# Kernel tuning notes

Hardware: AMD Instinct MI355X
Metric: run time of the kernel (lower is better)

## Reference

```python
import jax, jax.numpy as jnp
import numpy as np

D_MODEL = 768
H = 24            # nheads = d_inner / headdim
P = 64            # headdim
N = 64            # d_state (Mamba2Simple default)
DIN = 2 * D_MODEL             # expand=2 -> 1536
CONV_DIM = DIN + 2 * N        # 1664
DPROJ = 2 * DIN + 2 * N + H   # 3260
N_WRAPS = 8                   # 4 MambaFlipFlop layers x 2 MambaWrap each
IMG = 64 * 64
CHUNK = 128
EPS = 1e-5


def layer_norm(x, w, b):
    mu = jnp.mean(x, -1, keepdims=True)
    var = jnp.mean((x - mu) ** 2, -1, keepdims=True)
    return (x - mu) * jax.lax.rsqrt(var + EPS) * w + b


def segsum_exp(a):
    # a: [..., L] -> exp of segment sums, lower triangular (diag = 1)
    ac = jnp.cumsum(a, -1)
    d = ac[..., :, None] - ac[..., None, :]
    Lm = a.shape[-1]
    mask = jnp.tril(jnp.ones((Lm, Lm), bool))
    return jnp.exp(jnp.where(mask, d, -jnp.inf))


def ssd(X, A, Bm, Cm):
    # Chunked SSD (Mamba2). X:[b,t,h,p] (=x*dt), A:[b,t,h] (=dt*A_head),
    # Bm/Cm:[b,t,n] (ngroups=1, broadcast over heads).
    b, t, h, p = X.shape
    pad = (-t) % CHUNK
    X = jnp.pad(X, ((0, 0), (0, pad), (0, 0), (0, 0)))
    A = jnp.pad(A, ((0, 0), (0, pad), (0, 0)))
    Bm = jnp.pad(Bm, ((0, 0), (0, pad), (0, 0)))
    Cm = jnp.pad(Cm, ((0, 0), (0, pad), (0, 0)))
    c = (t + pad) // CHUNK
    X = X.reshape(b, c, CHUNK, h, p)
    A = A.reshape(b, c, CHUNK, h).transpose(0, 3, 1, 2)     # [b,h,c,l]
    Bm = Bm.reshape(b, c, CHUNK, N)
    Cm = Cm.reshape(b, c, CHUNK, N)
    Acs = jnp.cumsum(A, -1)                                  # [b,h,c,l]
    # intra-chunk (diagonal) block
    Lmat = segsum_exp(A)                                     # [b,h,c,l,l]
    G = jnp.einsum('bcln,bcsn->bcls', Cm, Bm)                # [b,c,l,s]
    M = G[:, None] * Lmat                                    # [b,h,c,l,s]
    Yd = jnp.einsum('bhcls,bcshp->bclhp', M, X)
    # chunk final states
    dec_st = jnp.exp(Acs[..., -1:] - Acs)                    # [b,h,c,l]
    states = jnp.einsum('bcln,bhcl,bclhp->bchpn', Bm, dec_st, X)
    states = jnp.concatenate([jnp.zeros_like(states[:, :1]), states], 1)
    chunk_sum = jnp.pad(Acs[..., -1], ((0, 0), (0, 0), (1, 0)))  # [b,h,c+1]
    dec_ch = segsum_exp(chunk_sum)                           # [b,h,c+1,c+1]
    states = jnp.einsum('bhzc,bchpn->bzhpn', dec_ch, states)[:, :-1]
    # state -> output (off-diagonal contribution)
    Yo = jnp.einsum('bcln,bchpn,bhcl->bclhp', Cm, states, jnp.exp(Acs))
    Y = (Yd + Yo).reshape(b, c * CHUNK, h, p)
    return Y[:, :t]


def mamba2(x, in_w, cw, cb, dtb, A_log, Dp, rmsw, ow):
    b, t, _ = x.shape
    zxbcdt = jnp.einsum('btd,ed->bte', x, in_w)              # [b,t,DPROJ]
    z = zxbcdt[..., :DIN]
    xBC = zxbcdt[..., DIN:DIN + CONV_DIM]
    dt = jax.nn.softplus(zxbcdt[..., -H:] + dtb)             # [b,t,H]
    # causal depthwise conv1d (kernel 4, pad left 3) + silu
    xBC = jax.lax.conv_general_dilated(
        xBC.transpose(0, 2, 1), cw, (1,), [(3, 0)],
        feature_group_count=CONV_DIM,
        dimension_numbers=('NCH', 'OIH', 'NCH')) + cb[None, :, None]
    xBC = jax.nn.silu(xBC).transpose(0, 2, 1)
    xh = xBC[..., :DIN].reshape(b, t, H, P)
    Bm = xBC[..., DIN:DIN + N]
    Cm = xBC[..., DIN + N:]
    A = -jnp.exp(A_log)                                      # [H]
    y = ssd(xh * dt[..., None], dt * A, Bm, Cm)
    y = y + Dp[None, None, :, None] * xh                     # D skip
    y = y.reshape(b, t, DIN)
    y = y * jax.nn.silu(z)                                   # gated RMSNorm
    y = y * jax.lax.rsqrt(jnp.mean(y * y, -1, keepdims=True) + EPS) * rmsw
    return jnp.einsum('btd,od->bto', y, ow)


def _model(im8, im64, from_rgb_w, from_rgb_b, to_rgb_w, to_rgb_b, s0, suffix,
           norm0_w, norm0_b, in_proj_w, conv1d_w, conv1d_b, dt_bias, A_log, Dp,
           rms_w, out_proj_w, ln_w, ln_b, lnc_w, lnc_b, conv2d_w, conv2d_b):
    b = im8.shape[0]
    e8 = im8 @ from_rgb_w.T + from_rgb_b                     # [b,64,D]
    z = e8.reshape(b, 8, 8, D_MODEL)                         # zoom 8x8 -> 64x64
    z = jnp.repeat(jnp.repeat(z, 8, 1), 8, 2).reshape(b, IMG, D_MODEL) + suffix
    x = jnp.concatenate([jnp.broadcast_to(s0, (b, 1, D_MODEL)), e8, z], 1)
    x = layer_norm(x, norm0_w, norm0_b)                      # [b,4161,D]

    def wrap(x, i):
        r = x
        h = layer_norm(x, ln_w[i], ln_b[i])
        h = mamba2(h, in_proj_w[i], conv1d_w[i], conv1d_b[i], dt_bias[i],
                   A_log[i], Dp[i], rms_w[i], out_proj_w[i])
        img = layer_norm(h[:, -IMG:], lnc_w[i], lnc_b[i]).reshape(b, 64, 64, D_MODEL)
        img = jax.lax.conv_general_dilated(
            img, conv2d_w[i], (1, 1), 'SAME',
            dimension_numbers=('NHWC', 'HWIO', 'NHWC')) + conv2d_b[i]
        h = jnp.concatenate([h[:, :-IMG], img.reshape(b, IMG, D_MODEL)], 1)
        return r + h

    def swap(x):  # reverse last IMG tokens (MambaFlipFlop.swap_order)
        return jnp.concatenate([x[:, :-IMG], jnp.flip(x[:, -IMG:], 1)], 1)

    for l in range(4):
        x = swap(wrap(x, 2 * l))
        x = swap(wrap(x, 2 * l + 1))
    y_hat = x[:, -IMG:] @ to_rgb_w.T + to_rgb_b              # [b,4096,3]
    loss = jnp.mean((y_hat - im64) ** 2)
    return y_hat, loss


def setup_inputs():
    key = jax.random.key(0)
    ks = jax.random.split(key, 16)
    rn = lambda k, s, sc=0.02: jax.random.normal(k, s, jnp.float32) * sc
    u = jax.random.uniform(ks[10], (N_WRAPS, H), minval=1e-3, maxval=0.1)
    return dict(
        im8=jax.random.normal(ks[0], (1, 64, 3), jnp.float32),
        im64=jax.random.normal(ks[1], (1, IMG, 3), jnp.float32),
        from_rgb_w=rn(ks[2], (D_MODEL, 3), 0.2),
        from_rgb_b=jnp.zeros((D_MODEL,), jnp.float32),
        to_rgb_w=rn(ks[3], (3, D_MODEL)),
        to_rgb_b=jnp.zeros((3,), jnp.float32),
        s0=rn(ks[4], (1, 1, D_MODEL), 1.0),
        suffix=rn(ks[5], (IMG, D_MODEL)),
        norm0_w=jnp.ones((D_MODEL,), jnp.float32),
        norm0_b=jnp.zeros((D_MODEL,), jnp.float32),
        in_proj_w=rn(ks[6], (N_WRAPS, DPROJ, D_MODEL)),
        conv1d_w=rn(ks[7], (N_WRAPS, CONV_DIM, 1, 4), 0.2),
        conv1d_b=jnp.zeros((N_WRAPS, CONV_DIM), jnp.float32),
        dt_bias=jnp.log(jnp.expm1(u)),
        A_log=jnp.log(jax.random.uniform(ks[11], (N_WRAPS, H), minval=1.0, maxval=16.0)),
        Dp=jnp.ones((N_WRAPS, H), jnp.float32),
        rms_w=jnp.ones((N_WRAPS, DIN), jnp.float32),
        out_proj_w=rn(ks[8], (N_WRAPS, D_MODEL, DIN)),
        ln_w=jnp.ones((N_WRAPS, D_MODEL), jnp.float32),
        ln_b=jnp.zeros((N_WRAPS, D_MODEL), jnp.float32),
        lnc_w=jnp.ones((N_WRAPS, D_MODEL), jnp.float32),
        lnc_b=jnp.zeros((N_WRAPS, D_MODEL), jnp.float32),
        conv2d_w=rn(ks[9], (N_WRAPS, 5, 5, D_MODEL, D_MODEL)),
        conv2d_b=jnp.zeros((N_WRAPS, D_MODEL), jnp.float32),
    )


def reference(im8, im64, from_rgb_w, from_rgb_b, to_rgb_w, to_rgb_b, s0, suffix,
              norm0_w, norm0_b, in_proj_w, conv1d_w, conv1d_b, dt_bias, A_log, Dp,
              rms_w, out_proj_w, ln_w, ln_b, lnc_w, lnc_b, conv2d_w, conv2d_b):
    return _model(im8, im64, from_rgb_w, from_rgb_b, to_rgb_w, to_rgb_b, s0, suffix,
                  norm0_w, norm0_b, in_proj_w, conv1d_w, conv1d_b, dt_bias, A_log, Dp,
                  rms_w, out_proj_w, ln_w, ln_b, lnc_w, lnc_b, conv2d_w, conv2d_b)
```

## Files before the change

kernel.cpp:

```cpp
#include <hip/hip_runtime.h>

#define D_MODEL 768
#define NH 24
#define HP 64
#define NSTATE 64
#define DIN 1536
#define CONV_DIM 1664
#define DPROJ 3224
#define TLEN 4161
#define IMG 4096
#define NCHUNK 33
#define CHUNK 128
#define TPAD (NCHUNK*CHUNK)
#define KCONV 19200

__device__ __forceinline__ float softplusf(float x) { return x > 20.f ? x : log1pf(expf(x)); }
__device__ __forceinline__ float siluf(float x) { return x / (1.f + expf(-x)); }

typedef __attribute__((ext_vector_type(8))) short short8v;
typedef __attribute__((ext_vector_type(4))) float ffrag;

__device__ __forceinline__ void splitf(float x, short& h, short& l) {
  unsigned u = __float_as_uint(x);
  unsigned r = (u + 0x7FFFu + ((u >> 16) & 1u)) & 0xFFFF0000u;
  h = (short)(r >> 16);
  float hf = __uint_as_float(r);
  float lof = x - hf;
  unsigned u2 = __float_as_uint(lof);
  unsigned r2 = u2 + 0x7FFFu + ((u2 >> 16) & 1u);
  l = (short)(r2 >> 16);
}

__device__ __forceinline__ void mfma_bf16(ffrag& c, short8v a, short8v b) {
  c = __builtin_amdgcn_mfma_f32_16x16x32_bf16(a, b, c, 0, 0, 0);
}

__global__ void e8_kernel(const float* __restrict__ im8, const float* __restrict__ w,
                          const float* __restrict__ b, float* __restrict__ e8) {
  int gid = blockIdx.x * blockDim.x + threadIdx.x;
  if (gid >= 64 * D_MODEL) return;
  int j = gid / D_MODEL, d = gid % D_MODEL;
  float acc = b[d];
  for (int c = 0; c < 3; c++) acc += im8[j * 3 + c] * w[d * 3 + c];
  e8[gid] = acc;
}

__global__ void build_x_kernel(const float* __restrict__ e8, const float* __restrict__ s0,
                               const float* __restrict__ suffix, float* __restrict__ out) {
  for (int gid = blockIdx.x * blockDim.x + threadIdx.x; gid < TLEN * D_MODEL;
       gid += gridDim.x * blockDim.x) {
    int t = gid / D_MODEL, d = gid % D_MODEL;
    float v;
    if (t == 0) v = s0[d];
    else if (t < 65) v = e8[(t - 1) * D_MODEL + d];
    else {
      int i = t - 65;
      int r = i >> 6, c = i & 63;
      v = e8[((r >> 3) * 8 + (c >> 3)) * D_MODEL + d] + suffix[(size_t)i * D_MODEL + d];
    }
    out[gid] = v;
  }
}

__global__ __launch_bounds__(256) void ln_kernel(const float* __restrict__ in,
                                                 const float* __restrict__ w, const float* __restrict__ b,
                                                 float* __restrict__ outf,
                                                 short* __restrict__ oh, short* __restrict__ ol,
                                                 int rows) {
  int r = blockIdx.x;
  if (r >= rows) return;
  const float* row = in + (size_t)r * D_MODEL;
  __shared__ float red[256];
  int tid = threadIdx.x;
  float v0 = row[tid], v1 = row[tid + 256], v2 = row[tid + 512];
  red[tid] = v0 + v1 + v2;
  __syncthreads();
  for (int o = 128; o; o >>= 1) { if (tid < o) red[tid] += red[tid + o]; __syncthreads(); }
  float mu = red[0] / (float)D_MODEL;
  __syncthreads();
  float d0 = v0 - mu, d1 = v1 - mu, d2 = v2 - mu;
  red[tid] = d0 * d0 + d1 * d1 + d2 * d2;
  __syncthreads();
  for (int o = 128; o; o >>= 1) { if (tid < o) red[tid] += red[tid + o]; __syncthreads(); }
  float inv = rsqrtf(red[0] / (float)D_MODEL + 1e-5f);
  float r0 = d0 * inv * w[tid] + b[tid];
  float r1 = d1 * inv * w[tid + 256] + b[tid + 256];
  float r2 = d2 * inv * w[tid + 512] + b[tid + 512];
  if (oh) {
    size_t base = (size_t)r * D_MODEL;
    short h, l;
    splitf(r0, h, l); oh[base + tid] = h; ol[base + tid] = l;
    splitf(r1, h, l); oh[base + tid + 256] = h; ol[base + tid + 256] = l;
    splitf(r2, h, l); oh[base + tid + 512] = h; ol[base + tid + 512] = l;
  } else {
    float* orow = outf + (size_t)r * D_MODEL;
    orow[tid] = r0; orow[tid + 256] = r1; orow[tid + 512] = r2;
  }
}

__global__ void split_mat_kernel(const float* __restrict__ src, short* __restrict__ hi,
                                 short* __restrict__ lo, int n) {
  for (int i = blockIdx.x * blockDim.x + threadIdx.x; i < n; i += gridDim.x * blockDim.x) {
    short h, l; splitf(src[i], h, l);
    hi[i] = h; lo[i] = l;
  }
}

__global__ __launch_bounds__(256) void split_convw_kernel(const float* __restrict__ W,
                                                          short* __restrict__ hi,
                                                          short* __restrict__ lo) {
  __shared__ float t[32][33];
  int tap = blockIdx.x;
  int ic0 = blockIdx.y * 32, oc0 = blockIdx.z * 32;
  int tid = threadIdx.x;
  #pragma unroll
  for (int e = 0; e < 4; e++) {
    int idx = tid + e * 256;
    int r = idx >> 5, c = idx & 31;
    t[r][c] = W[((size_t)tap * 768 + ic0 + r) * 768 + oc0 + c];
  }
  __syncthreads();
  #pragma unroll
  for (int e = 0; e < 4; e++) {
    int idx = tid + e * 256;
    int r = idx & 31, c = idx >> 5;
    short h, l; splitf(t[r][c], h, l);
    size_t o = (size_t)(oc0 + c) * KCONV + (size_t)tap * 768 + ic0 + r;
    hi[o] = h; lo[o] = l;
  }
}

template<int CONV>
__global__ __launch_bounds__(256, 2) void mm_bf16(
    const short* __restrict__ Ah, const short* __restrict__ Al,
    const short* __restrict__ Bh, const short* __restrict__ Bl,
    float* __restrict__ C, float* __restrict__ Cpart,
    int M, int N, int K, int ldb) {
  __shared__ __align__(16) short AsH[128 * 64];
  __shared__ __align__(16) short AsL[128 * 64];
  __shared__ __align__(16) short BsH[128 * 64];
  __shared__ __align__(16) short BsL[128 * 64];
  const int bm = blockIdx.x * 128;
  const int bn = blockIdx.y * 128;
  const int tid = threadIdx.x;
  const int lane = tid & 63;
  const int wid = tid >> 6;
  const int wm = (wid >> 1) * 64, wn = (wid & 1) * 64;
  const int lm = lane & 15, lk = lane >> 4;
  const int tap0 = CONV ? blockIdx.z * 5 : 0;
  const int nsteps = CONV ? 5 * 12 : K / 64;
  float* Cout = C;
  if (CONV && blockIdx.z > 0) Cout = Cpart + (size_t)(blockIdx.z - 1) * IMG * D_MODEL;
  const short8v ZV = {0, 0, 0, 0, 0, 0, 0, 0};

  short8v sAh[4], sAl[4], sBh[4], sBl[4];
  int s_row[4], s_kc[4];
  #pragma unroll
  for (int e = 0; e < 4; e++) { int id = tid + e * 256; s_row[e] = id >> 3; s_kc[e] = id & 7; }

  auto stage = [&](int step) {
    int k0, tap = 0;
    if (CONV) { tap = tap0 + step / 12; k0 = (step % 12) * 64; }
    else k0 = step * 64;
    #pragma unroll
    for (int e = 0; e < 4; e++) {
      int row = s_row[e], kc = s_kc[e];
      bool av; size_t aoff;
      if (CONV) {
        int px = bm + row;
        int r = (px >> 6) + tap / 5 - 2;
        int c = (px & 63) + tap % 5 - 2;
        av = (r >= 0 && r < 64 && c >= 0 && c < 64);
        aoff = (size_t)(r * 64 + c) * 768 + k0 + kc * 8;
      } else {
        int gm = bm + row;
        av = gm < M;
        aoff = (size_t)gm * K + k0 + kc * 8;
      }
      sAh[e] = av ? *(const short8v*)(Ah + aoff) : ZV;
      sAl[e] = av ? *(const short8v*)(Al + aoff) : ZV;
      int gn = bn + row;
      bool bv = gn < N;
      size_t boff = (size_t)gn * ldb + (CONV ? tap * 768 : 0) + k0 + kc * 8;
      sBh[e] = bv ? *(const short8v*)(Bh + boff) : ZV;
      sBl[e] = bv ? *(const short8v*)(Bl + boff) : ZV;
    }
  };

  auto lds_write = [&]() {
    #pragma unroll
    for (int e = 0; e < 4; e++) {
      int row = s_row[e];
      int off = row * 64 + ((s_kc[e] ^ (row & 7)) * 8);
      *(short8v*)(AsH + off) = sAh[e];
      *(short8v*)(AsL + off) = sAl[e];
      *(short8v*)(BsH + off) = sBh[e];
      *(short8v*)(BsL + off) = sBl[e];
    }
  };

  ffrag acc[4][4];
  const ffrag FZ = {0.f, 0.f, 0.f, 0.f};
  #pragma unroll
  for (int i = 0; i < 4; i++)
    #pragma unroll
    for (int j = 0; j < 4; j++) acc[i][j] = FZ;

  auto compute = [&]() {
    #pragma unroll
    for (int ks = 0; ks < 2; ks++) {
      short8v ahf[4], alf[4], bhf[4], blf[4];
      #pragma unroll
      for (int i = 0; i < 4; i++) {
        int ra = wm + i * 16 + lm;
        int oa = ra * 64 + (((lk + 4 * ks) ^ (ra & 7)) * 8);
        ahf[i] = *(const short8v*)(AsH + oa);
        alf[i] = *(const short8v*)(AsL + oa);
        int rb = wn + i * 16 + lm;
        int ob = rb * 64 + (((lk + 4 * ks) ^ (rb & 7)) * 8);
        bhf[i] = *(const short8v*)(BsH + ob);
        blf[i] = *(const short8v*)(BsL + ob);
      }
      #pragma unroll
      for (int i = 0; i < 4; i++)
        #pragma unroll
        for (int j = 0; j < 4; j++) {
          mfma_bf16(acc[i][j], ahf[i], bhf[j]);
          mfma_bf16(acc[i][j], ahf[i], blf[j]);
          mfma_bf16(acc[i][j], alf[i], bhf[j]);
        }
    }
  };

  stage(0);
  lds_write();
  __syncthreads();
  for (int step = 0; step < nsteps; ++step) {
    bool more = step + 1 < nsteps;
    if (more) stage(step + 1);
    compute();
    __syncthreads();
    if (more) { lds_write(); __syncthreads(); }
  }

  #pragma unroll
  for (int i = 0; i < 4; i++) {
    #pragma unroll
    for (int r = 0; r < 4; r++) {
      int row = bm + wm + i * 16 + lk * 4 + r;
      if (row >= M) continue;
      #pragma unroll
      for (int j = 0; j < 4; j++) {
        int col = bn + wn + j * 16 + lm;
        if (col < N) Cout[(size_t)row * N + col] = acc[i][j][r];
      }
    }
  }
}

__global__ void conv_reduce_kernel(float* __restrict__ dst, const float* __restrict__ part,
                                   const float* __restrict__ bias) {
  for (int gid = blockIdx.x * blockDim.x + threadIdx.x; gid < IMG * D_MODEL;
       gid += gridDim.x * blockDim.x) {
    float s = dst[gid] + bias[gid % D_MODEL];
    #pragma unroll
    for (int p = 0; p < 4; p++) s += part[(size_t)p * IMG * D_MODEL + gid];
    dst[gid] = s;
  }
}

__global__ void conv1d_kernel(const float* __restrict__ zx, const float* __restrict__ cw,
                              const float* __restrict__ cb, float* __restrict__ xBC) {
  for (int gid = blockIdx.x * blockDim.x + threadIdx.x; gid < TLEN * CONV_DIM;
       gid += gridDim.x * blockDim.x) {
    int t = gid / CONV_DIM, ch = gid % CONV_DIM;
    float acc = cb[ch];
    #pragma unroll
    for (int k = 0; k < 4; k++) {
      int tt = t - 3 + k;
      if (tt >= 0) acc += zx[(size_t)tt * DPROJ + DIN + ch] * cw[ch * 4 + k];
    }
    xBC[gid] = siluf(acc);
  }
}

__global__ void dt_kernel(const float* __restrict__ zx, const float* __restrict__ dt_bias,
                          float* __restrict__ dt) {
  for (int gid = blockIdx.x * blockDim.x + threadIdx.x; gid < TLEN * NH;
       gid += gridDim.x * blockDim.x) {
    int t = gid / NH, h = gid % NH;
    float v = zx[(size_t)t * DPROJ + DPROJ - NH + h] + dt_bias[h];
    dt[gid] = softplusf(v);
  }
}

__global__ void acs_kernel(const float* __restrict__ dt, const float* __restrict__ A_log,
                           float* __restrict__ Acs, float* __restrict__ csum) {
  int gid = blockIdx.x * blockDim.x + threadIdx.x;
  if (gid >= NCHUNK * NH) return;
  int c = gid / NH, h = gid % NH;
  float A = -expf(A_log[h]);
  float acc = 0.f;
  for (int l = 0; l < CHUNK; l++) {
    int t = c * CHUNK + l;
    float a = (t < TLEN) ? dt[(size_t)t * NH + h] * A : 0.f;
    acc += a;
    Acs[(size_t)(c * CHUNK + l) * NH + h] = acc;
  }
  csum[c * NH + h] = acc;
}

__global__ __launch_bounds__(256) void chunk_state_kernel(const float* __restrict__ xBC,
                                                          const float* __restrict__ dt,
                                                          const float* __restrict__ Acs,
                                                          const float* __restrict__ csum,
                                                          float* __restrict__ cstate) {
  int c = blockIdx.x, h = blockIdx.y;
  __shared__ float Bs[CHUNK][NSTATE];
  __shared__ float Xs[CHUNK][HP];
  int tid = threadIdx.x;
  float cs = csum[c * NH + h];
  for (int idx = tid; idx < CHUNK * 64; idx += 256) {
    int l = idx >> 6, n = idx & 63;
    int t = c * CHUNK + l;
    if (t < TLEN) {
      float a = Acs[(size_t)t * NH + h];
      Bs[l][n] = xBC[(size_t)t * CONV_DIM + DIN + n];
      Xs[l][n] = xBC[(size_t)t * CONV_DIM + h * HP + n] * dt[(size_t)t * NH + h] * expf(cs - a);
    } else { Bs[l][n] = 0.f; Xs[l][n] = 0.f; }
  }
  __syncthreads();
  int pt = (tid >> 4) * 4, nt = (tid & 15) * 4;
  float acc[4][4] = {};
  for (int l = 0; l < CHUNK; l++) {
    float xv[4], bv[4];
    #pragma unroll
    for (int i = 0; i < 4; i++) xv[i] = Xs[l][pt + i];
    #pragma unroll
    for (int j = 0; j < 4; j++) bv[j] = Bs[l][nt + j];
    #pragma unroll
    for (int i = 0; i < 4; i++)
      #pragma unroll
      for (int j = 0; j < 4; j++) acc[i][j] += xv[i] * bv[j];
  }
  size_t base = (((size_t)c * NH) + h) * 64 * 64;
  for (int i = 0; i < 4; i++)
    for (int j = 0; j < 4; j++)
      cstate[base + (size_t)(pt + i) * 64 + nt + j] = acc[i][j];
}

__global__ __launch_bounds__(256) void state_scan_kernel(const float* __restrict__ cstate,
                                                         const float* __restrict__ csum,
                                                         float* __restrict__ sstate) {
  int h = blockIdx.x;
  int tid = threadIdx.x;
  float S[16];
  #pragma unroll
  for (int j = 0; j < 16; j++) S[j] = 0.f;
  for (int z = 0; z < NCHUNK; z++) {
    size_t base = (((size_t)z * NH) + h) * 4096;
    float dec = expf(csum[z * NH + h]);
    #pragma unroll
    for (int j = 0; j < 16; j++) {
      int idx = j * 256 + tid;
      sstate[base + idx] = S[j];
      S[j] = S[j] * dec + cstate[base + idx];
    }
  }
}

__global__ __launch_bounds__(256, 1) void ssd_y_kernel(const float* __restrict__ xBC,
                                                       const float* __restrict__ dt,
                                                       const float* __restrict__ Acs,
                                                       const float* __restrict__ sstate,
                                                       const float* __restrict__ Dp,
                                                       float* __restrict__ y) {
  int c = blockIdx.x, h = blockIdx.y;
  __shared__ float Cs[CHUNK][NSTATE];
  __shared__ float Bx[CHUNK][NSTATE];
  __shared__ float Gm[CHUNK][CHUNK];
  __shared__ float Ash[CHUNK];
  int tid = threadIdx.x;
  for (int idx = tid; idx < CHUNK * 64; idx += 256) {
    int l = idx >> 6, n = idx & 63;
    int t = c * CHUNK + l;
    bool v = t < TLEN;
    Cs[l][n] = v ? xBC[(size_t)t * CONV_DIM + DIN + NSTATE + n] : 0.f;
    Bx[l][n] = v ? xBC[(size_t)t * CONV_DIM + DIN + n] : 0.f;
  }
  if (tid < CHUNK) Ash[tid] = Acs[(size_t)(c * CHUNK + tid) * NH + h];
  __syncthreads();
  {
    int lt = (tid >> 4) * 8, st = (tid & 15) * 8;
    float acc[8][8] = {};
    for (int n = 0; n < 64; n++) {
      float cv[8], bv[8];
      #pragma unroll
      for (int i = 0; i < 8; i++) cv[i] = Cs[lt + i][n];
      #pragma unroll
      for (int j = 0; j < 8; j++) bv[j] = Bx[st + j][n];
      #pragma unroll
      for (int i = 0; i < 8; i++)
        #pragma unroll
        for (int j = 0; j < 8; j++) acc[i][j] += cv[i] * bv[j];
    }
    for (int i = 0; i < 8; i++)
      for (int j = 0; j < 8; j++) {
        int l = lt + i, s = st + j;
        Gm[l][s] = (s <= l) ? acc[i][j] * expf(Ash[l] - Ash[s]) : 0.f;
      }
  }
  __syncthreads();
  for (int idx = tid; idx < CHUNK * 64; idx += 256) {
    int l = idx >> 6, p = idx & 63;
    int t = c * CHUNK + l;
    Bx[l][p] = (t < TLEN) ? xBC[(size_t)t * CONV_DIM + h * HP + p] * dt[(size_t)t * NH + h] : 0.f;
  }
  __syncthreads();
  int lt = (tid >> 4) * 8, pt = (tid & 15) * 4;
  float yd[8][4] = {};
  for (int s = 0; s < CHUNK; s++) {
    float m8[8], x4[4];
    #pragma unroll
    for (int i = 0; i < 8; i++) m8[i] = Gm[lt + i][s];
    #pragma unroll
    for (int j = 0; j < 4; j++) x4[j] = Bx[s][pt + j];
    #pragma unroll
    for (int i = 0; i < 8; i++)
      #pragma unroll
      for (int j = 0; j < 4; j++) yd[i][j] += m8[i] * x4[j];
  }
  __syncthreads();
  for (int idx = tid; idx < 64 * 64; idx += 256) {
    int p = idx >> 6, n = idx & 63;
    Bx[p][n] = sstate[(((size_t)c * NH) + h) * 4096 + idx];
  }
  __syncthreads();
  float yo[8][4] = {};
  for (int n = 0; n < 64; n++) {
    float c8[8], s4[4];
    #pragma unroll
    for (int i = 0; i < 8; i++) c8[i] = Cs[lt + i][n];
    #pragma unroll
    for (int j = 0; j < 4; j++) s4[j] = Bx[pt + j][n];
    #pragma unroll
    for (int i = 0; i < 8; i++)
      #pragma unroll
      for (int j = 0; j < 4; j++) yo[i][j] += c8[i] * s4[j];
  }
  float dph = Dp[h];
  for (int i = 0; i < 8; i++) {
    int l = lt + i, t = c * CHUNK + l;
    if (t >= TLEN) continue;
    float ea = expf(Ash[l]);
    for (int j = 0; j < 4; j++) {
      int p = pt + j;
      float xh = xBC[(size_t)t * CONV_DIM + h * HP + p];
      y[(size_t)t * DIN + h * HP + p] = yd[i][j] + ea * yo[i][j] + dph * xh;
    }
  }
}

__global__ __launch_bounds__(256) void gate_rms_kernel(const float* __restrict__ y,
                                                       const float* __restrict__ zx,
                                                       const float* __restrict__ rms_w,
                                                       short* __restrict__ oh,
                                                       short* __restrict__ ol) {
  int t = blockIdx.x;
  if (t >= TLEN) return;
  __shared__ float red[256];
  int tid = threadIdx.x;
  float v[6];
  float ss = 0.f;
  #pragma unroll
  for (int e = 0; e < 6; e++) {
    int d = e * 256 + tid;
    float z = zx[(size_t)t * DPROJ + d];
    float val = y[(size_t)t * DIN + d] * siluf(z);
    v[e] = val;
    ss += val * val;
  }
  red[tid] = ss;
  __syncthreads();
  for (int o = 128; o; o >>= 1) { if (tid < o) red[tid] += red[tid + o]; __syncthreads(); }
  float scale = rsqrtf(red[0] / (float)DIN + 1e-5f);
  #pragma unroll
  for (int e = 0; e < 6; e++) {
    int d = e * 256 + tid;
    short h, l;
    splitf(v[e] * scale * rms_w[d], h, l);
    oh[(size_t)t * DIN + d] = h;
    ol[(size_t)t * DIN + d] = l;
  }
}

__global__ void resadd_flip_kernel(const float* __restrict__ x, const float* __restrict__ hbuf,
                                   float* __restrict__ xnew) {
  for (int gid = blockIdx.x * blockDim.x + threadIdx.x; gid < TLEN * D_MODEL;
       gid += gridDim.x * blockDim.x) {
    int t = gid / D_MODEL, d = gid % D_MODEL;
    int st = (t < 65) ? t : 65 + (IMG - 1 - (t - 65));
    size_t sidx = (size_t)st * D_MODEL + d;
    xnew[gid] = x[sidx] + hbuf[sidx];
  }
}

__global__ void zero_loss_kernel(float* loss) { *loss = 0.f; }

__global__ void head_kernel(const float* __restrict__ ximg, const float* __restrict__ w,
                            const float* __restrict__ b, const float* __restrict__ im64,
                            float* __restrict__ out, float* __restrict__ loss_acc) {
  int p = blockIdx.x;
  int lane = threadIdx.x;
  const float* row = ximg + (size_t)p * D_MODEL;
  float a0 = 0.f, a1 = 0.f, a2 = 0.f;
  for (int d = lane; d < D_MODEL; d += 64) {
    float xv = row[d];
    a0 += xv * w[d];
    a1 += xv * w[D_MODEL + d];
    a2 += xv * w[2 * D_MODEL + d];
  }
  for (int off = 32; off; off >>= 1) {
    a0 += __shfl_down(a0, off);
    a1 += __shfl_down(a1, off);
    a2 += __shfl_down(a2, off);
  }
  if (lane == 0) {
    a0 += b[0]; a1 += b[1]; a2 += b[2];
    out[p * 3 + 0] = a0;
    out[p * 3 + 1] = a1;
    out[p * 3 + 2] = a2;
    float e0 = a0 - im64[p * 3 + 0];
    float e1 = a1 - im64[p * 3 + 1];
    float e2 = a2 - im64[p * 3 + 2];
    atomicAdd(loss_acc, e0 * e0 + e1 * e1 + e2 * e2);
  }
}

__global__ void finalize_loss_kernel(const float* __restrict__ loss_acc, float* __restrict__ out) {
  out[IMG * 3] = loss_acc[0] / (float)(IMG * 3);
}

extern "C" void kernel_launch(void* const* d_in, const int* in_sizes, int n_in,
                              void* d_out, int out_size, void* d_ws, size_t ws_size,
                              hipStream_t stream) {
  const float* im8       = (const float*)d_in[0];
  const float* im64      = (const float*)d_in[1];
  const float* from_rgb_w= (const float*)d_in[2];
  const float* from_rgb_b= (const float*)d_in[3];
  const float* to_rgb_w  = (const float*)d_in[4];
  const float* to_rgb_b  = (const float*)d_in[5];
  const float* s0        = (const float*)d_in[6];
  const float* suffix    = (const float*)d_in[7];
  const float* norm0_w   = (const float*)d_in[8];
  const float* norm0_b   = (const float*)d_in[9];
  const float* in_proj_w = (const float*)d_in[10];
  const float* conv1d_w  = (const float*)d_in[11];
  const float* conv1d_b  = (const float*)d_in[12];
  const float* dt_bias   = (const float*)d_in[13];
  const float* A_log     = (const float*)d_in[14];
  const float* Dp        = (const float*)d_in[15];
  const float* rms_w     = (const float*)d_in[16];
  const float* out_proj_w= (const float*)d_in[17];
  const float* ln_w      = (const float*)d_in[18];
  const float* ln_b      = (const float*)d_in[19];
  const float* lnc_w     = (const float*)d_in[20];
  const float* lnc_b     = (const float*)d_in[21];
  const float* conv2d_w  = (const float*)d_in[22];
  const float* conv2d_b  = (const float*)d_in[23];

  float* W = (float*)d_ws;
  size_t off = 0;
  auto alloc = [&](size_t n) { float* p = W + off; off += (n + 3) & ~(size_t)3; return p; };
  auto salloc = [&](size_t n) { return (short*)alloc((n + 1) / 2); };
  float* xA     = alloc((size_t)TLEN * D_MODEL);
  float* xB     = alloc((size_t)TLEN * D_MODEL);
  float* hbuf   = alloc((size_t)TLEN * D_MODEL);
  float* zx     = alloc((size_t)TLEN * DPROJ);
  float* xBC    = alloc((size_t)TLEN * CONV_DIM);
  float* dtb    = alloc((size_t)TLEN * NH);
  float* Acs    = alloc((size_t)TPAD * NH);
  float* csum   = alloc((size_t)NCHUNK * NH);
  float* ybuf   = alloc((size_t)TLEN * DIN);
  float* cstate = alloc((size_t)NCHUNK * NH * 64 * 64);
  float* sstate = alloc((size_t)NCHUNK * NH * 64 * 64);
  float* e8     = alloc((size_t)64 * D_MODEL);
  float* lossp  = alloc(4);
  short* xs_h   = salloc((size_t)TLEN * D_MODEL);
  short* xs_l   = salloc((size_t)TLEN * D_MODEL);
  short* ybs_h  = salloc((size_t)TLEN * DIN);
  short* ybs_l  = salloc((size_t)TLEN * DIN);
  short* img_h  = salloc((size_t)IMG * D_MODEL);
  short* img_l  = salloc((size_t)IMG * D_MODEL);
  short* wA_h   = salloc((size_t)DPROJ * D_MODEL);
  short* wA_l   = salloc((size_t)DPROJ * D_MODEL);
  short* wO_h   = salloc((size_t)D_MODEL * DIN);
  short* wO_l   = salloc((size_t)D_MODEL * DIN);
  short* wC_h   = (short*)xBC;
  short* wC_l   = wC_h + (size_t)D_MODEL * KCONV;
  (void)ws_size; (void)in_sizes; (void)n_in; (void)out_size;

  float* outp = (float*)d_out;

  e8_kernel<<<(64 * D_MODEL + 255) / 256, 256, 0, stream>>>(im8, from_rgb_w, from_rgb_b, e8);
  build_x_kernel<<<2048, 256, 0, stream>>>(e8, s0, suffix, xB);
  ln_kernel<<<TLEN, 256, 0, stream>>>(xB, norm0_w, norm0_b, xA, nullptr, nullptr, TLEN);

  float* x = xA;
  float* xn = xB;
  for (int i = 0; i < 8; i++) {
    const float* ipw = in_proj_w + (size_t)i * DPROJ * D_MODEL;
    const float* cw  = conv1d_w + (size_t)i * CONV_DIM * 4;
    const float* cb  = conv1d_b + (size_t)i * CONV_DIM;
    const float* dtbias_i = dt_bias + (size_t)i * NH;
    const float* alog_i   = A_log + (size_t)i * NH;
    const float* dp_i     = Dp + (size_t)i * NH;
    const float* rmsw_i   = rms_w + (size_t)i * DIN;
    const float* opw      = out_proj_w + (size_t)i * D_MODEL * DIN;
    const float* lnw_i    = ln_w + (size_t)i * D_MODEL;
    const float* lnb_i    = ln_b + (size_t)i * D_MODEL;
    const float* lncw_i   = lnc_w + (size_t)i * D_MODEL;
    const float* lncb_i   = lnc_b + (size_t)i * D_MODEL;
    const float* c2w      = conv2d_w + (size_t)i * 25 * D_MODEL * D_MODEL;
    const float* c2b      = conv2d_b + (size_t)i * D_MODEL;

    split_mat_kernel<<<1024, 256, 0, stream>>>(ipw, wA_h, wA_l, DPROJ * D_MODEL);
    split_mat_kernel<<<1024, 256, 0, stream>>>(opw, wO_h, wO_l, D_MODEL * DIN);

    ln_kernel<<<TLEN, 256, 0, stream>>>(x, lnw_i, lnb_i, nullptr, xs_h, xs_l, TLEN);
    mm_bf16<0><<<dim3(33, 26), 256, 0, stream>>>(xs_h, xs_l, wA_h, wA_l, zx, nullptr,
                                                 TLEN, DPROJ, D_MODEL, D_MODEL);
    conv1d_kernel<<<4096, 256, 0, stream>>>(zx, cw, cb, xBC);
    dt_kernel<<<(TLEN * NH + 255) / 256, 256, 0, stream>>>(zx, dtbias_i, dtb);
    acs_kernel<<<(NCHUNK * NH + 255) / 256, 256, 0, stream>>>(dtb, alog_i, Acs, csum);
    chunk_state_kernel<<<dim3(NCHUNK, NH), 256, 0, stream>>>(xBC, dtb, Acs, csum, cstate);
    state_scan_kernel<<<NH, 256, 0, stream>>>(cstate, csum, sstate);
    ssd_y_kernel<<<dim3(NCHUNK, NH), 256, 0, stream>>>(xBC, dtb, Acs, sstate, dp_i, ybuf);
    gate_rms_kernel<<<TLEN, 256, 0, stream>>>(ybuf, zx, rmsw_i, ybs_h, ybs_l);
    split_convw_kernel<<<dim3(25, 24, 24), 256, 0, stream>>>(c2w, wC_h, wC_l);
    mm_bf16<0><<<dim3(33, 6), 256, 0, stream>>>(ybs_h, ybs_l, wO_h, wO_l, hbuf, nullptr,
                                                TLEN, D_MODEL, DIN, DIN);
    ln_kernel<<<IMG, 256, 0, stream>>>(hbuf + (size_t)65 * D_MODEL, lncw_i, lncb_i,
                                       nullptr, img_h, img_l, IMG);
    mm_bf16<1><<<dim3(32, 6, 5), 256, 0, stream>>>(img_h, img_l, wC_h, wC_l,
                                                   hbuf + (size_t)65 * D_MODEL, zx,
                                                   IMG, D_MODEL, 768, KCONV);
    conv_reduce_kernel<<<2048, 256, 0, stream>>>(hbuf + (size_t)65 * D_MODEL, zx, c2b);
    resadd_flip_kernel<<<2048, 256, 0, stream>>>(x, hbuf, xn);
    float* tmp = x; x = xn; xn = tmp;
  }

  zero_loss_kernel<<<1, 1, 0, stream>>>(lossp);
  head_kernel<<<IMG, 64, 0, stream>>>(x + (size_t)65 * D_MODEL, to_rgb_w, to_rgb_b, im64,
                                      outp, lossp);
  finalize_loss_kernel<<<1, 1, 0, stream>>>(lossp, outp);
}
```

Baseline: 8.848 ms.

## Rewrite bf16x3 GEMM with direct-to-LDS double buffering and zero-padded conv input

The split-bf16 GEMM now loads tiles straight from global memory into LDS with global_load_lds, alternating between two LDS buffers so the next K-slice loads while the current one computes. It switches from 16x16x32 to 32x32x16 MFMA and uses 32-wide K steps. The conv2d input is written into a zero-padded 68x68 image so the implicit-im2col loads need no bounds checks. The SSD inner loops are also vectorised with float4 LDS reads. Bounds guards on A/B loads are gone, so edge tiles now read past the logical matrix ends into neighbouring buffers; only the stores stay guarded.

```diff
diff --git a/kernel.cpp b/kernel.cpp
--- a/kernel.cpp
+++ b/kernel.cpp
@@ -13,12 +13,14 @@
 #define CHUNK 128
 #define TPAD (NCHUNK*CHUNK)
 #define KCONV 19200
+#define IMGP (68*68)
 
 __device__ __forceinline__ float softplusf(float x) { return x > 20.f ? x : log1pf(expf(x)); }
 __device__ __forceinline__ float siluf(float x) { return x / (1.f + expf(-x)); }
 
 typedef __attribute__((ext_vector_type(8))) short short8v;
-typedef __attribute__((ext_vector_type(4))) float ffrag;
+typedef __attribute__((ext_vector_type(4))) float f4;
+typedef __attribute__((ext_vector_type(16))) float f32x16;
 
 __device__ __forceinline__ void splitf(float x, short& h, short& l) {
   unsigned u = __float_as_uint(x);
@@ -31,8 +33,13 @@
   l = (short)(r2 >> 16);
 }
 
-__device__ __forceinline__ void mfma_bf16(ffrag& c, short8v a, short8v b) {
-  c = __builtin_amdgcn_mfma_f32_16x16x32_bf16(a, b, c, 0, 0, 0);
+__device__ __forceinline__ f32x16 mfma32(short8v a, short8v b, f32x16 c) {
+  return __builtin_amdgcn_mfma_f32_32x32x16_bf16(a, b, c, 0, 0, 0);
+}
+
+__device__ __forceinline__ void gld16(const short* g, const short* l) {
+  __builtin_amdgcn_global_load_lds((const __attribute__((address_space(1))) void*)g,
+                                   (__attribute__((address_space(3))) void*)l, 16, 0, 0);
 }
 
 __global__ void e8_kernel(const float* __restrict__ im8, const float* __restrict__ w,
@@ -62,11 +69,16 @@
   }
 }
 
+__global__ void zero_pair_kernel(short* __restrict__ a, short* __restrict__ b, int n) {
+  for (int gid = blockIdx.x * blockDim.x + threadIdx.x; gid < n;
+       gid += gridDim.x * blockDim.x) { a[gid] = 0; b[gid] = 0; }
+}
+
 __global__ __launch_bounds__(256) void ln_kernel(const float* __restrict__ in,
                                                  const float* __restrict__ w, const float* __restrict__ b,
                                                  float* __restrict__ outf,
                                                  short* __restrict__ oh, short* __restrict__ ol,
-                                                 int rows) {
+                                                 int rows, int pad68) {
   int r = blockIdx.x;
   if (r >= rows) return;
   const float* row = in + (size_t)r * D_MODEL;
@@ -87,7 +99,8 @@
   float r1 = d1 * inv * w[tid + 256] + b[tid + 256];
   float r2 = d2 * inv * w[tid + 512] + b[tid + 512];
   if (oh) {
-    size_t base = (size_t)r * D_MODEL;
+    size_t rr = pad68 ? (size_t)(((r >> 6) + 2) * 68 + (r & 63) + 2) : (size_t)r;
+    size_t base = rr * D_MODEL;
     short h, l;
     splitf(r0, h, l); oh[base + tid] = h; ol[base + tid] = l;
     splitf(r1, h, l); oh[base + tid + 256] = h; ol[base + tid + 256] = l;
@@ -136,123 +149,105 @@
     const short* __restrict__ Bh, const short* __restrict__ Bl,
     float* __restrict__ C, float* __restrict__ Cpart,
     int M, int N, int K, int ldb) {
-  __shared__ __align__(16) short AsH[128 * 64];
-  __shared__ __align__(16) short AsL[128 * 64];
-  __shared__ __align__(16) short BsH[128 * 64];
-  __shared__ __align__(16) short BsL[128 * 64];
+  __shared__ __align__(16) short AsH[2][128 * 32];
+  __shared__ __align__(16) short AsL[2][128 * 32];
+  __shared__ __align__(16) short BsH[2][128 * 32];
+  __shared__ __align__(16) short BsL[2][128 * 32];
   const int bm = blockIdx.x * 128;
   const int bn = blockIdx.y * 128;
   const int tid = threadIdx.x;
   const int lane = tid & 63;
-  const int wid = tid >> 6;
-  const int wm = (wid >> 1) * 64, wn = (wid & 1) * 64;
-  const int lm = lane & 15, lk = lane >> 4;
+  const int wv = tid >> 6;
+  const int wm = (wv >> 1) * 64, wn = (wv & 1) * 64;
+  const int l31 = lane & 31, lh = lane >> 5;
   const int tap0 = CONV ? blockIdx.z * 5 : 0;
-  const int nsteps = CONV ? 5 * 12 : K / 64;
+  const int nsteps = CONV ? 120 : K / 32;
   float* Cout = C;
   if (CONV && blockIdx.z > 0) Cout = Cpart + (size_t)(blockIdx.z - 1) * IMG * D_MODEL;
-  const short8v ZV = {0, 0, 0, 0, 0, 0, 0, 0};
-
-  short8v sAh[4], sAl[4], sBh[4], sBl[4];
-  int s_row[4], s_kc[4];
-  #pragma unroll
-  for (int e = 0; e < 4; e++) { int id = tid + e * 256; s_row[e] = id >> 3; s_kc[e] = id & 7; }
-
-  auto stage = [&](int step) {
-    int k0, tap = 0;
-    if (CONV) { tap = tap0 + step / 12; k0 = (step % 12) * 64; }
-    else k0 = step * 64;
-    #pragma unroll
-    for (int e = 0; e < 4; e++) {
-      int row = s_row[e], kc = s_kc[e];
-      bool av; size_t aoff;
+
+  const int srow = lane >> 2;
+  const int schunk = lane & 3;
+
+  auto stage = [&](int tap, int k0, int buf) {
+    int dr = 0, dc = 0;
+    if (CONV) { dr = tap / 5; dc = tap % 5; }
+    #pragma unroll
+    for (int half = 0; half < 2; half++) {
+      int rb = wv * 32 + half * 16;
+      int row = rb + srow;
+      int kc = schunk ^ (row & 3);
+      size_t aoff;
       if (CONV) {
         int px = bm + row;
-        int r = (px >> 6) + tap / 5 - 2;
-        int c = (px & 63) + tap % 5 - 2;
-        av = (r >= 0 && r < 64 && c >= 0 && c < 64);
-        aoff = (size_t)(r * 64 + c) * 768 + k0 + kc * 8;
+        aoff = (size_t)(((px >> 6) + dr) * 68 + (px & 63) + dc) * 768 + k0 + kc * 8;
       } else {
-        int gm = bm + row;
-        av = gm < M;
-        aoff = (size_t)gm * K + k0 + kc * 8;
+        aoff = (size_t)(bm + row) * K + k0 + kc * 8;
       }
-      sAh[e] = av ? *(const short8v*)(Ah + aoff) : ZV;
-      sAl[e] = av ? *(const short8v*)(Al + aoff) : ZV;
-      int gn = bn + row;
-      bool bv = gn < N;
-      size_t boff = (size_t)gn * ldb + (CONV ? tap * 768 : 0) + k0 + kc * 8;
-      sBh[e] = bv ? *(const short8v*)(Bh + boff) : ZV;
-      sBl[e] = bv ? *(const short8v*)(Bl + boff) : ZV;
+      gld16(Ah + aoff, &AsH[buf][rb * 32]);
+      gld16(Al + aoff, &AsL[buf][rb * 32]);
+      size_t boff = (size_t)(bn + row) * ldb + (CONV ? tap * 768 : 0) + k0 + kc * 8;
+      gld16(Bh + boff, &BsH[buf][rb * 32]);
+      gld16(Bl + boff, &BsL[buf][rb * 32]);
     }
   };
 
-  auto lds_write = [&]() {
-    #pragma unroll
-    for (int e = 0; e < 4; e++) {
-      int row = s_row[e];
-      int off = row * 64 + ((s_kc[e] ^ (row & 7)) * 8);
-      *(short8v*)(AsH + off) = sAh[e];
-      *(short8v*)(AsL + off) = sAl[e];
-      *(short8v*)(BsH + off) = sBh[e];
-      *(short8v*)(BsL + off) = sBl[e];
+  const f32x16 FZ = {};
+  f32x16 acc[2][2];
+  #pragma unroll
+  for (int i = 0; i < 2; i++)
+    #pragma unroll
+    for (int j = 0; j < 2; j++) acc[i][j] = FZ;
+
+  auto compute = [&](int buf) {
+    #pragma unroll
+    for (int ks = 0; ks < 2; ks++) {
+      int kc = ks * 2 + lh;
+      short8v ah[2], al[2], bh[2], bl[2];
+      #pragma unroll
+      for (int i = 0; i < 2; i++) {
+        int ra = wm + i * 32 + l31;
+        int oa = ra * 32 + ((kc ^ (ra & 3)) * 8);
+        ah[i] = *(const short8v*)&AsH[buf][oa];
+        al[i] = *(const short8v*)&AsL[buf][oa];
+        int rb = wn + i * 32 + l31;
+        int ob = rb * 32 + ((kc ^ (rb & 3)) * 8);
+        bh[i] = *(const short8v*)&BsH[buf][ob];
+        bl[i] = *(const short8v*)&BsL[buf][ob];
+      }
+      #pragma unroll
+      for (int i = 0; i < 2; i++)
+        #pragma unroll
+        for (int j = 0; j < 2; j++) {
+          acc[i][j] = mfma32(ah[i], bh[j], acc[i][j]);
+          acc[i][j] = mfma32(ah[i], bl[j], acc[i][j]);
+          acc[i][j] = mfma32(al[i], bh[j], acc[i][j]);
+        }
     }
   };
 
-  ffrag acc[4][4];
-  const ffrag FZ = {0.f, 0.f, 0.f, 0.f};
+  int nt_tap = tap0, nt_k0 = 0;
+  stage(nt_tap, nt_k0, 0);
+  nt_k0 += 32; if (CONV && nt_k0 == 768) { nt_k0 = 0; nt_tap++; }
+  asm volatile("s_waitcnt vmcnt(0)\n\ts_barrier" ::: "memory");
+  for (int t = 0; t < nsteps; ++t) {
+    if (t + 1 < nsteps) {
+      stage(nt_tap, nt_k0, (t + 1) & 1);
+      nt_k0 += 32; if (CONV && nt_k0 == 768) { nt_k0 = 0; nt_tap++; }
+    }
+    compute(t & 1);
+    asm volatile("s_waitcnt vmcnt(0)\n\ts_barrier" ::: "memory");
+  }
+
   #pragma unroll
-  for (int i = 0; i < 4; i++)
-    #pragma unroll
-    for (int j = 0; j < 4; j++) acc[i][j] = FZ;
-
-  auto compute = [&]() {
-    #pragma unroll
-    for (int ks = 0; ks < 2; ks++) {
-      short8v ahf[4], alf[4], bhf[4], blf[4];
-      #pragma unroll
-      for (int i = 0; i < 4; i++) {
-        int ra = wm + i * 16 + lm;
-        int oa = ra * 64 + (((lk + 4 * ks) ^ (ra & 7)) * 8);
-        ahf[i] = *(const short8v*)(AsH + oa);
-        alf[i] = *(const short8v*)(AsL + oa);
-        int rb = wn + i * 16 + lm;
-        int ob = rb * 64 + (((lk + 4 * ks) ^ (rb & 7)) * 8);
-        bhf[i] = *(const short8v*)(BsH + ob);
-        blf[i] = *(const short8v*)(BsL + ob);
-      }
-      #pragma unroll
-      for (int i = 0; i < 4; i++)
-        #pragma unroll
-        for (int j = 0; j < 4; j++) {
-          mfma_bf16(acc[i][j], ahf[i], bhf[j]);
-          mfma_bf16(acc[i][j], ahf[i], blf[j]);
-          mfma_bf16(acc[i][j], alf[i], bhf[j]);
-        }
-    }
-  };
-
-  stage(0);
-  lds_write();
-  __syncthreads();
-  for (int step = 0; step < nsteps; ++step) {
-    bool more = step + 1 < nsteps;
-    if (more) stage(step + 1);
-    compute();
-    __syncthreads();
-    if (more) { lds_write(); __syncthreads(); }
-  }
-
-  #pragma unroll
-  for (int i = 0; i < 4; i++) {
-    #pragma unroll
-    for (int r = 0; r < 4; r++) {
-      int row = bm + wm + i * 16 + lk * 4 + r;
-      if (row >= M) continue;
-      #pragma unroll
-      for (int j = 0; j < 4; j++) {
-        int col = bn + wn + j * 16 + lm;
-        if (col < N) Cout[(size_t)row * N + col] = acc[i][j][r];
+  for (int i = 0; i < 2; i++) {
+    #pragma unroll
+    for (int r = 0; r < 16; r++) {
+      int grow = bm + wm + i * 32 + (r & 3) + 8 * (r >> 2) + 4 * lh;
+      if (grow >= M) continue;
+      #pragma unroll
+      for (int j = 0; j < 2; j++) {
+        int gcol = bn + wn + j * 32 + l31;
+        if (gcol < N) Cout[(size_t)grow * N + gcol] = acc[i][j][r];
       }
     }
   }
@@ -393,16 +388,18 @@
   {
     int lt = (tid >> 4) * 8, st = (tid & 15) * 8;
     float acc[8][8] = {};
-    for (int n = 0; n < 64; n++) {
-      float cv[8], bv[8];
-      #pragma unroll
-      for (int i = 0; i < 8; i++) cv[i] = Cs[lt + i][n];
-      #pragma unroll
-      for (int j = 0; j < 8; j++) bv[j] = Bx[st + j][n];
+    for (int n0 = 0; n0 < 64; n0 += 4) {
+      f4 cv[8], bv[8];
+      #pragma unroll
+      for (int i = 0; i < 8; i++) cv[i] = *(const f4*)&Cs[lt + i][n0];
+      #pragma unroll
+      for (int j = 0; j < 8; j++) bv[j] = *(const f4*)&Bx[st + j][n0];
       #pragma unroll
       for (int i = 0; i < 8; i++)
         #pragma unroll
-        for (int j = 0; j < 8; j++) acc[i][j] += cv[i] * bv[j];
+        for (int j = 0; j < 8; j++)
+          acc[i][j] += cv[i][0] * bv[j][0] + cv[i][1] * bv[j][1]
+                     + cv[i][2] * bv[j][2] + cv[i][3] * bv[j][3];
     }
     for (int i = 0; i < 8; i++)
       for (int j = 0; j < 8; j++) {
@@ -419,16 +416,18 @@
   __syncthreads();
   int lt = (tid >> 4) * 8, pt = (tid & 15) * 4;
   float yd[8][4] = {};
-  for (int s = 0; s < CHUNK; s++) {
-    float m8[8], x4[4];
-    #pragma unroll
-    for (int i = 0; i < 8; i++) m8[i] = Gm[lt + i][s];
-    #pragma unroll
-    for (int j = 0; j < 4; j++) x4[j] = Bx[s][pt + j];
+  for (int s0 = 0; s0 < CHUNK; s0 += 4) {
+    f4 m4[8], xr[4];
+    #pragma unroll
+    for (int i = 0; i < 8; i++) m4[i] = *(const f4*)&Gm[lt + i][s0];
+    #pragma unroll
+    for (int u = 0; u < 4; u++) xr[u] = *(const f4*)&Bx[s0 + u][pt];
     #pragma unroll
     for (int i = 0; i < 8; i++)
       #pragma unroll
-      for (int j = 0; j < 4; j++) yd[i][j] += m8[i] * x4[j];
+      for (int j = 0; j < 4; j++)
+        yd[i][j] += m4[i][0] * xr[0][j] + m4[i][1] * xr[1][j]
+                  + m4[i][2] * xr[2][j] + m4[i][3] * xr[3][j];
   }
   __syncthreads();
   for (int idx = tid; idx < 64 * 64; idx += 256) {
@@ -437,16 +436,18 @@
   }
   __syncthreads();
   float yo[8][4] = {};
-  for (int n = 0; n < 64; n++) {
-    float c8[8], s4[4];
-    #pragma unroll
-    for (int i = 0; i < 8; i++) c8[i] = Cs[lt + i][n];
-    #pragma unroll
-    for (int j = 0; j < 4; j++) s4[j] = Bx[pt + j][n];
+  for (int n0 = 0; n0 < 64; n0 += 4) {
+    f4 c4[8], sv[4];
+    #pragma unroll
+    for (int i = 0; i < 8; i++) c4[i] = *(const f4*)&Cs[lt + i][n0];
+    #pragma unroll
+    for (int j = 0; j < 4; j++) sv[j] = *(const f4*)&Bx[pt + j][n0];
     #pragma unroll
     for (int i = 0; i < 8; i++)
       #pragma unroll
-      for (int j = 0; j < 4; j++) yo[i][j] += c8[i] * s4[j];
+      for (int j = 0; j < 4; j++)
+        yo[i][j] += c4[i][0] * sv[j][0] + c4[i][1] * sv[j][1]
+                  + c4[i][2] * sv[j][2] + c4[i][3] * sv[j][3];
   }
   float dph = Dp[h];
   for (int i = 0; i < 8; i++) {
@@ -590,8 +591,8 @@
   short* xs_l   = salloc((size_t)TLEN * D_MODEL);
   short* ybs_h  = salloc((size_t)TLEN * DIN);
   short* ybs_l  = salloc((size_t)TLEN * DIN);
-  short* img_h  = salloc((size_t)IMG * D_MODEL);
-  short* img_l  = salloc((size_t)IMG * D_MODEL);
+  short* img_h  = salloc((size_t)IMGP * D_MODEL);
+  short* img_l  = salloc((size_t)IMGP * D_MODEL);
   short* wA_h   = salloc((size_t)DPROJ * D_MODEL);
   short* wA_l   = salloc((size_t)DPROJ * D_MODEL);
   short* wO_h   = salloc((size_t)D_MODEL * DIN);
@@ -604,7 +605,8 @@
 
   e8_kernel<<<(64 * D_MODEL + 255) / 256, 256, 0, stream>>>(im8, from_rgb_w, from_rgb_b, e8);
   build_x_kernel<<<2048, 256, 0, stream>>>(e8, s0, suffix, xB);
-  ln_kernel<<<TLEN, 256, 0, stream>>>(xB, norm0_w, norm0_b, xA, nullptr, nullptr, TLEN);
+  ln_kernel<<<TLEN, 256, 0, stream>>>(xB, norm0_w, norm0_b, xA, nullptr, nullptr, TLEN, 0);
+  zero_pair_kernel<<<2048, 256, 0, stream>>>(img_h, img_l, IMGP * D_MODEL);
 
   float* x = xA;
   float* xn = xB;
@@ -627,7 +629,7 @@
     split_mat_kernel<<<1024, 256, 0, stream>>>(ipw, wA_h, wA_l, DPROJ * D_MODEL);
     split_mat_kernel<<<1024, 256, 0, stream>>>(opw, wO_h, wO_l, D_MODEL * DIN);
 
-    ln_kernel<<<TLEN, 256, 0, stream>>>(x, lnw_i, lnb_i, nullptr, xs_h, xs_l, TLEN);
+    ln_kernel<<<TLEN, 256, 0, stream>>>(x, lnw_i, lnb_i, nullptr, xs_h, xs_l, TLEN, 0);
     mm_bf16<0><<<dim3(33, 26), 256, 0, stream>>>(xs_h, xs_l, wA_h, wA_l, zx, nullptr,
                                                  TLEN, DPROJ, D_MODEL, D_MODEL);
     conv1d_kernel<<<4096, 256, 0, stream>>>(zx, cw, cb, xBC);
@@ -641,7 +643,7 @@
     mm_bf16<0><<<dim3(33, 6), 256, 0, stream>>>(ybs_h, ybs_l, wO_h, wO_l, hbuf, nullptr,
                                                 TLEN, D_MODEL, DIN, DIN);
     ln_kernel<<<IMG, 256, 0, stream>>>(hbuf + (size_t)65 * D_MODEL, lncw_i, lncb_i,
-                                       nullptr, img_h, img_l, IMG);
+                                       nullptr, img_h, img_l, IMG, 1);
     mm_bf16<1><<<dim3(32, 6, 5), 256, 0, stream>>>(img_h, img_l, wC_h, wC_l,
                                                    hbuf + (size_t)65 * D_MODEL, zx,
                                                    IMG, D_MODEL, 768, KCONV);
```

New measurement: 10.57 ms. 1.2x slower.
